# Kernel optimization log

Hardware: AMD Instinct MI355X
Metric: run time of the kernel (lower is better)

The kernel has to match this reference:

```python
import jax, jax.numpy as jnp
import numpy as np

DIM = 1024
HEAD_NUM = 8
D_HEAD = DIM // HEAD_NUM
B, S = 4, 2048


def setup_inputs() -> dict:
    key = jax.random.key(0)
    ks = jax.random.split(key, 7)
    scale = 0.02
    return {
        "Q": jax.random.normal(ks[0], (B, S, DIM), dtype=jnp.float32),
        "K": jax.random.normal(ks[1], (B, S, DIM), dtype=jnp.float32),
        "V": jax.random.normal(ks[2], (B, S, DIM), dtype=jnp.float32),
        "W_Q": jax.random.normal(ks[3], (DIM, DIM), dtype=jnp.float32) * scale,
        "W_K": jax.random.normal(ks[4], (DIM, DIM), dtype=jnp.float32) * scale,
        "W_V": jax.random.normal(ks[5], (DIM, DIM), dtype=jnp.float32) * scale,
        "W_O": jax.random.normal(ks[6], (DIM, DIM), dtype=jnp.float32) * scale,
    }


def reference(Q, K, V, W_Q, W_K, W_V, W_O):
    # torch nn.Linear(bias=False): y = x @ W.T
    b, s, d = Q.shape
    h, dh = HEAD_NUM, d // HEAD_NUM

    def proj_split(x, W):
        # split_head: tensor_split along feature dim into h contiguous chunks,
        # stack at dim 1 -> [b, h, s, dh]; equivalent to reshape+transpose.
        y = jnp.einsum('bsd,ed->bse', x, W)
        return y.reshape(b, s, h, dh).transpose(0, 2, 1, 3)

    q = proj_split(Q, W_Q)  # [b,h,s,dh]
    k = proj_split(K, W_K)
    v = proj_split(V, W_V)

    scores = jnp.einsum('bhqd,bhkd->bhqk', q, k) / jnp.sqrt(jnp.float32(dh))
    # FAITHFUL to original: nn.Softmax(dim=1) normalizes over the HEAD axis.
    attn = jax.nn.softmax(scores, axis=1)
    # dropout is identity in eval mode
    ctx = jnp.einsum('bhqk,bhkd->bhqd', attn, v)  # [b,h,s,dh]
    # concat_head: heads concatenated back along feature dim in order
    ctx = ctx.transpose(0, 2, 1, 3).reshape(b, s, d)
    return jnp.einsum('bsd,ed->bse', ctx, W_O)
```

## Files before the change

### kernel.cpp

```cpp
#include <hip/hip_runtime.h>
#include <math.h>
#include <stdint.h>


typedef __attribute__((ext_vector_type(8))) __bf16 bf16x8;
typedef __attribute__((ext_vector_type(4))) __bf16 bf16x4;
typedef __attribute__((ext_vector_type(4))) float  f32x4;

__device__ __forceinline__ f32x4 mfma16(bf16x8 a, bf16x8 b, f32x4 c) {
    return __builtin_amdgcn_mfma_f32_16x16x32_bf16(a, b, c, 0, 0, 0);
}

__device__ __forceinline__ void cp16(void* lds, const void* g) {
    __builtin_amdgcn_global_load_lds(
        (__attribute__((address_space(1))) void*)(void*)(const_cast<void*>(g)),
        (__attribute__((address_space(3))) void*)lds,
        16, 0, 0);
}

__global__ void cast_f32_to_bf16(const float* __restrict__ src,
                                 __bf16* __restrict__ dst, int n4) {
    int i = blockIdx.x * blockDim.x + threadIdx.x;
    const int stride = gridDim.x * blockDim.x;
    for (; i < n4; i += stride) {
        float4 f = ((const float4*)src)[i];
        bf16x4 o;
        o[0] = (__bf16)f.x; o[1] = (__bf16)f.y; o[2] = (__bf16)f.z; o[3] = (__bf16)f.w;
        ((bf16x4*)dst)[i] = o;
    }
}

__global__ void cast4_f32_to_bf16(const float* __restrict__ s0, __bf16* __restrict__ d0,
                                  const float* __restrict__ s1, __bf16* __restrict__ d1,
                                  const float* __restrict__ s2, __bf16* __restrict__ d2,
                                  const float* __restrict__ s3, __bf16* __restrict__ d3,
                                  int n4) {
    const float* s = (blockIdx.y == 0) ? s0 : (blockIdx.y == 1) ? s1
                    : (blockIdx.y == 2) ? s2 : s3;
    __bf16* d = (blockIdx.y == 0) ? d0 : (blockIdx.y == 1) ? d1
               : (blockIdx.y == 2) ? d2 : d3;
    int i = blockIdx.x * blockDim.x + threadIdx.x;
    const int stride = gridDim.x * blockDim.x;
    for (; i < n4; i += stride) {
        float4 f = ((const float4*)s)[i];
        bf16x4 o;
        o[0] = (__bf16)f.x; o[1] = (__bf16)f.y; o[2] = (__bf16)f.z; o[3] = (__bf16)f.w;
        ((bf16x4*)d)[i] = o;
    }
}

template<int MODE>
__global__ __launch_bounds__(256, 2) void gemm_bt(const __bf16* __restrict__ A,
                                                  const __bf16* __restrict__ Bt,
                                                  void* __restrict__ out,
                                                  float scale)
{
    __shared__ __bf16 As[128 * 32];
    __shared__ __bf16 Bs[128 * 32];
    const int tid  = threadIdx.x;
    const int lane = tid & 63;
    const int u = lane >> 4, v = lane & 15;
    const int w = tid >> 6;
    const int wm = (w >> 1) * 64, wn = (w & 1) * 64;
    const long tM = (long)blockIdx.y * 128;
    const int  tN = blockIdx.x * 128;

    f32x4 acc[4][4];
#pragma unroll
    for (int i = 0; i < 4; ++i)
#pragma unroll
        for (int j = 0; j < 4; ++j) acc[i][j] = (f32x4){0.f, 0.f, 0.f, 0.f};

    const int c0 = tid, c1 = tid + 256;
    const int ar0 = c0 >> 2, ak0 = (c0 & 3) * 8;
    const int ar1 = c1 >> 2, ak1 = (c1 & 3) * 8;

    const __bf16* Ab = A  + tM * 1024;
    const __bf16* Bb = Bt + (long)tN * 1024;

    for (int k0 = 0; k0 < 1024; k0 += 32) {
        __syncthreads();
        cp16(&As[ar0 * 32 + ak0], Ab + (long)ar0 * 1024 + k0 + ak0);
        cp16(&As[ar1 * 32 + ak1], Ab + (long)ar1 * 1024 + k0 + ak1);
        cp16(&Bs[ar0 * 32 + ak0], Bb + (long)ar0 * 1024 + k0 + ak0);
        cp16(&Bs[ar1 * 32 + ak1], Bb + (long)ar1 * 1024 + k0 + ak1);
        __syncthreads();

        bf16x8 af[4], bfr[4];
#pragma unroll
        for (int i = 0; i < 4; ++i)
            af[i] = *(const bf16x8*)&As[(wm + i * 16 + v) * 32 + u * 8];
#pragma unroll
        for (int j = 0; j < 4; ++j)
            bfr[j] = *(const bf16x8*)&Bs[(wn + j * 16 + v) * 32 + u * 8];
#pragma unroll
        for (int i = 0; i < 4; ++i)
#pragma unroll
            for (int j = 0; j < 4; ++j)
                acc[i][j] = mfma16(af[i], bfr[j], acc[i][j]);
    }

#pragma unroll
    for (int i = 0; i < 4; ++i) {
#pragma unroll
        for (int j = 0; j < 4; ++j) {
            const long row0 = tM + wm + i * 16 + u * 4;
            const int  col  = tN + wn + j * 16 + v;
            if (MODE == 0) {
                __bf16* o = (__bf16*)out;
#pragma unroll
                for (int r = 0; r < 4; ++r)
                    o[(row0 + r) * 1024 + col] = (__bf16)(acc[i][j][r] * scale);
            } else if (MODE == 1) {
                float* o = (float*)out;
#pragma unroll
                for (int r = 0; r < 4; ++r)
                    o[(row0 + r) * 1024 + col] = acc[i][j][r];
            } else {
                __bf16* o = (__bf16*)out;
                const int bidx = (int)(row0 >> 11);
                const int s    = (int)(row0 & 2047);
                const int h = col >> 7, dh = col & 127;
                bf16x4 pk;
#pragma unroll
                for (int r = 0; r < 4; ++r) pk[r] = (__bf16)acc[i][j][r];
                *(bf16x4*)&o[((long)(bidx * 8 + h) * 128 + dh) * 2048 + s] = pk;
            }
        }
    }
}

struct QkSm {
    union {
        struct { __bf16 As[64 * 32]; __bf16 Bs[128 * 32]; } s;
        __bf16 tb[128 * 68];
    };
};
__global__ __launch_bounds__(256, 2) void qk_head_softmax(
    const __bf16* __restrict__ kp, const __bf16* __restrict__ qp,
    __bf16* __restrict__ P, int b_base, int q_base)
{
    __shared__ QkSm sm;
    const int tid  = threadIdx.x;
    const int lane = tid & 63;
    const int u = lane >> 4, v = lane & 15;
    const int w = tid >> 6;
    const int wm = (w >> 1) * 32, wn = (w & 1) * 64;
    const int bloc = blockIdx.z;
    const int b    = b_base + bloc;
    const int k0   = blockIdx.x * 64;
    const int q0l  = blockIdx.y * 128;
    const int q0g  = q_base + q0l;
    const long Cq  = (long)gridDim.y * 128;

    const int ar0 = tid >> 2, ak0 = (tid & 3) * 8;
    const int ar1 = ar0 + 64, ak1 = ak0;

    const __bf16* Ka = kp + ((long)b * 2048 + k0) * 1024;
    const __bf16* Qa = qp + ((long)b * 2048 + q0g) * 1024;

    f32x4 den[2][4];
#pragma unroll
    for (int i = 0; i < 2; ++i)
#pragma unroll
        for (int j = 0; j < 4; ++j) den[i][j] = (f32x4){0.f, 0.f, 0.f, 0.f};

    bf16x4 e8[8][2][4];

#pragma unroll
    for (int h = 0; h < 8; ++h) {
        f32x4 acc[2][4];
#pragma unroll
        for (int i = 0; i < 2; ++i)
#pragma unroll
            for (int j = 0; j < 4; ++j) acc[i][j] = (f32x4){0.f, 0.f, 0.f, 0.f};

#pragma unroll
        for (int kb = 0; kb < 4; ++kb) {
            const int co = h * 128 + kb * 32;
            __syncthreads();
            cp16(&sm.s.As[ar0 * 32 + ak0], Ka + (long)ar0 * 1024 + co + ak0);
            cp16(&sm.s.Bs[ar0 * 32 + ak0], Qa + (long)ar0 * 1024 + co + ak0);
            cp16(&sm.s.Bs[ar1 * 32 + ak1], Qa + (long)ar1 * 1024 + co + ak1);
            __syncthreads();

            bf16x8 af[2], bfr[4];
#pragma unroll
            for (int i = 0; i < 2; ++i)
                af[i] = *(const bf16x8*)&sm.s.As[(wm + i * 16 + v) * 32 + u * 8];
#pragma unroll
            for (int j = 0; j < 4; ++j)
                bfr[j] = *(const bf16x8*)&sm.s.Bs[(wn + j * 16 + v) * 32 + u * 8];
#pragma unroll
            for (int i = 0; i < 2; ++i)
#pragma unroll
                for (int j = 0; j < 4; ++j)
                    acc[i][j] = mfma16(af[i], bfr[j], acc[i][j]);
        }
#pragma unroll
        for (int i = 0; i < 2; ++i)
#pragma unroll
            for (int j = 0; j < 4; ++j) {
                bf16x4 pk;
#pragma unroll
                for (int r = 0; r < 4; ++r) {
                    float e = __expf(acc[i][j][r]);
                    den[i][j][r] += e;
                    pk[r] = (__bf16)e;
                }
                e8[h][i][j] = pk;
            }
    }

    f32x4 rinv[2][4];
#pragma unroll
    for (int i = 0; i < 2; ++i)
#pragma unroll
        for (int j = 0; j < 4; ++j)
#pragma unroll
            for (int r = 0; r < 4; ++r) rinv[i][j][r] = 1.0f / den[i][j][r];

#pragma unroll
    for (int h = 0; h < 8; ++h) {
        __syncthreads();
#pragma unroll
        for (int i = 0; i < 2; ++i)
#pragma unroll
            for (int j = 0; j < 4; ++j) {
                const int kc = wm + i * 16 + u * 4;
                const int qr = wn + j * 16 + v;
                bf16x4 t = e8[h][i][j];
                bf16x4 o;
#pragma unroll
                for (int r = 0; r < 4; ++r)
                    o[r] = (__bf16)((float)t[r] * rinv[i][j][r]);
                *(bf16x4*)&sm.tb[qr * 68 + kc] = o;
            }
        __syncthreads();
        __bf16* Ph = P + ((long)(bloc * 8 + h) * Cq + q0l) * 2048 + k0;
#pragma unroll
        for (int p = 0; p < 4; ++p) {
            const int qq = p * 32 + (tid >> 3);
            const int kk = (tid & 7) * 8;
            *(bf16x8*)&Ph[(long)qq * 2048 + kk] = *(const bf16x8*)&sm.tb[qq * 68 + kk];
        }
    }
}

__global__ __launch_bounds__(256, 2) void pv_gemm(
    const __bf16* __restrict__ vt, const __bf16* __restrict__ P,
    __bf16* __restrict__ ctx, int b_base, int q_base)
{
    __shared__ __bf16 As[128 * 32];
    __shared__ __bf16 Bs[128 * 32];
    const int tid  = threadIdx.x;
    const int lane = tid & 63;
    const int u = lane >> 4, v = lane & 15;
    const int w = tid >> 6;
    const int wm = (w >> 1) * 64, wn = (w & 1) * 64;
    const int bhl  = blockIdx.y;
    const int bloc = bhl >> 3, h = bhl & 7;
    const int b    = b_base + bloc;
    const int q0l  = blockIdx.x * 128;
    const int q0g  = q_base + q0l;
    const long Cq  = (long)gridDim.x * 128;

    const int c0 = tid, c1 = tid + 256;
    const int ar0 = c0 >> 2, ak0 = (c0 & 3) * 8;
    const int ar1 = c1 >> 2, ak1 = (c1 & 3) * 8;

    const __bf16* Ab = vt + (long)(b * 8 + h) * 128 * 2048;
    const __bf16* Bb = P  + ((long)(bloc * 8 + h) * Cq + q0l) * 2048;

    f32x4 acc[4][4];
#pragma unroll
    for (int i = 0; i < 4; ++i)
#pragma unroll
        for (int j = 0; j < 4; ++j) acc[i][j] = (f32x4){0.f, 0.f, 0.f, 0.f};

    for (int k0 = 0; k0 < 2048; k0 += 32) {
        __syncthreads();
        cp16(&As[ar0 * 32 + ak0], Ab + (long)ar0 * 2048 + k0 + ak0);
        cp16(&As[ar1 * 32 + ak1], Ab + (long)ar1 * 2048 + k0 + ak1);
        cp16(&Bs[ar0 * 32 + ak0], Bb + (long)ar0 * 2048 + k0 + ak0);
        cp16(&Bs[ar1 * 32 + ak1], Bb + (long)ar1 * 2048 + k0 + ak1);
        __syncthreads();

        bf16x8 af[4], bfr[4];
#pragma unroll
        for (int i = 0; i < 4; ++i)
            af[i] = *(const bf16x8*)&As[(wm + i * 16 + v) * 32 + u * 8];
#pragma unroll
        for (int j = 0; j < 4; ++j)
            bfr[j] = *(const bf16x8*)&Bs[(wn + j * 16 + v) * 32 + u * 8];
#pragma unroll
        for (int i = 0; i < 4; ++i)
#pragma unroll
            for (int j = 0; j < 4; ++j)
                acc[i][j] = mfma16(af[i], bfr[j], acc[i][j]);
    }

#pragma unroll
    for (int i = 0; i < 4; ++i) {
#pragma unroll
        for (int j = 0; j < 4; ++j) {
            const int dh0 = wm + i * 16 + u * 4;
            const int q   = q0g + wn + j * 16 + v;
            bf16x4 pk;
#pragma unroll
            for (int r = 0; r < 4; ++r) pk[r] = (__bf16)acc[i][j][r];
            *(bf16x4*)&ctx[((long)b * 2048 + q) * 1024 + h * 128 + dh0] = pk;
        }
    }
}

__global__ __launch_bounds__(256, 2) void attn_softmax_head(
    const __bf16* __restrict__ qp, const __bf16* __restrict__ kp,
    const __bf16* __restrict__ vt, __bf16* __restrict__ ctx)
{
    __shared__ float part[8 * 256];
    __shared__ float pb[4][2][16 * 33];

    const int tid  = threadIdx.x;
    const int lane = tid & 63;
    const int w = tid >> 6;
    const int u = lane >> 4, v = lane & 15;
    const int b  = blockIdx.y;
    const int q0 = blockIdx.x * 16;

    const long qoff = ((long)b * 2048 + q0 + v) * 1024;
    bf16x8 qf[2][4];
#pragma unroll
    for (int hh = 0; hh < 2; ++hh) {
        const int h = 2 * w + hh;
#pragma unroll
        for (int kk = 0; kk < 4; ++kk)
            qf[hh][kk] = *(const bf16x8*)(qp + qoff + h * 128 + kk * 32 + u * 8);
    }

    f32x4 acc[2][8];
#pragma unroll
    for (int hh = 0; hh < 2; ++hh)
#pragma unroll
        for (int dt = 0; dt < 8; ++dt) acc[hh][dt] = (f32x4){0.f, 0.f, 0.f, 0.f};

    for (int kt = 0; kt < 2048; kt += 32) {
        float e[2][2][4];
#pragma unroll
        for (int hh = 0; hh < 2; ++hh) {
            const int h = 2 * w + hh;
#pragma unroll
            for (int t = 0; t < 2; ++t) {
                f32x4 s = (f32x4){0.f, 0.f, 0.f, 0.f};
                const __bf16* kb = kp + ((long)b * 2048 + kt + t * 16 + v) * 1024
                                      + h * 128 + u * 8;
#pragma unroll
                for (int kk = 0; kk < 4; ++kk)
                    s = mfma16(*(const bf16x8*)(kb + kk * 32), qf[hh][kk], s);
#pragma unroll
                for (int r = 0; r < 4; ++r) e[hh][t][r] = __expf(s[r]);
            }
        }
#pragma unroll
        for (int t = 0; t < 2; ++t)
#pragma unroll
            for (int r = 0; r < 4; ++r)
                part[(t * 4 + r) * 256 + w * 64 + lane] = e[0][t][r] + e[1][t][r];
        __syncthreads();
#pragma unroll
        for (int t = 0; t < 2; ++t)
#pragma unroll
            for (int r = 0; r < 4; ++r) {
                const int j = (t * 4 + r) * 256 + lane;
                const float den = part[j] + part[j + 64] + part[j + 128] + part[j + 192];
                const float rinv = 1.0f / den;
                const int kl = t * 16 + u * 4 + r;
                pb[w][0][v * 33 + kl] = e[0][t][r] * rinv;
                pb[w][1][v * 33 + kl] = e[1][t][r] * rinv;
            }
        bf16x8 pf[2];
#pragma unroll
        for (int hh = 0; hh < 2; ++hh)
#pragma unroll
            for (int jj = 0; jj < 8; ++jj)
                pf[hh][jj] = (__bf16)pb[w][hh][v * 33 + u * 8 + jj];
#pragma unroll
        for (int hh = 0; hh < 2; ++hh) {
            const int h = 2 * w + hh;
            const __bf16* vb = vt + ((long)(b * 8 + h) * 128 + v) * 2048 + kt + u * 8;
#pragma unroll
            for (int dt = 0; dt < 8; ++dt)
                acc[hh][dt] = mfma16(*(const bf16x8*)(vb + (long)dt * 16 * 2048),
                                     pf[hh], acc[hh][dt]);
        }
        __syncthreads();
    }

#pragma unroll
    for (int hh = 0; hh < 2; ++hh) {
        const int h = 2 * w + hh;
#pragma unroll
        for (int dt = 0; dt < 8; ++dt) {
            bf16x4 o;
#pragma unroll
            for (int r = 0; r < 4; ++r) o[r] = (__bf16)acc[hh][dt][r];
            *(bf16x4*)(ctx + ((long)b * 2048 + q0 + v) * 1024
                           + h * 128 + dt * 16 + u * 4) = o;
        }
    }
}

extern "C" void kernel_launch(void* const* d_in, const int* in_sizes, int n_in,
                              void* d_out, int out_size, void* d_ws, size_t ws_size,
                              hipStream_t stream)
{
    const float* Q  = (const float*)d_in[0];
    const float* K  = (const float*)d_in[1];
    const float* V  = (const float*)d_in[2];
    const float* WQ = (const float*)d_in[3];
    const float* WK = (const float*)d_in[4];
    const float* WV = (const float*)d_in[5];
    const float* WO = (const float*)d_in[6];

    __bf16* ws = (__bf16*)d_ws;
    __bf16* wq = ws;
    __bf16* wk = wq + 1048576;
    __bf16* wv = wk + 1048576;
    __bf16* wo = wv + 1048576;
    __bf16* xb = wo + 1048576;
    __bf16* qp = xb + 8388608;
    __bf16* kp = qp + 8388608;
    __bf16* vt = kp + 8388608;
    __bf16* pbuf = vt + 8388608;

    const float qscale = 0.08838834764831845f;

    cast4_f32_to_bf16<<<dim3(256, 4), 256, 0, stream>>>(
        WQ, wq, WK, wk, WV, wv, WO, wo, 262144);

    dim3 gg(8, 64), gb(256);
    cast_f32_to_bf16<<<4096, 256, 0, stream>>>(Q, xb, 2097152);
    gemm_bt<0><<<gg, gb, 0, stream>>>(xb, wq, qp, qscale);
    cast_f32_to_bf16<<<4096, 256, 0, stream>>>(K, xb, 2097152);
    gemm_bt<0><<<gg, gb, 0, stream>>>(xb, wk, kp, 1.0f);
    cast_f32_to_bf16<<<4096, 256, 0, stream>>>(V, xb, 2097152);
    gemm_bt<2><<<gg, gb, 0, stream>>>(xb, wv, vt, 1.0f);

    const size_t baseBytes = 37748736ULL * 2ULL;
    const size_t avail = (ws_size > baseBytes) ? ws_size - baseBytes : 0;
    const int cfgs[6][2] = {{4,2048},{2,2048},{1,2048},{1,1024},{1,512},{1,256}};
    int nb = 0, C = 0;
    for (int c = 0; c < 6; ++c) {
        const size_t need = (size_t)cfgs[c][0] * 8 * cfgs[c][1] * 2048 * 2;
        if (need <= avail) { nb = cfgs[c][0]; C = cfgs[c][1]; break; }
    }

    if (nb) {
        for (int bb = 0; bb < 4; bb += nb)
            for (int qq = 0; qq < 2048; qq += C) {
                qk_head_softmax<<<dim3(32, C / 128, nb), gb, 0, stream>>>(
                    kp, qp, pbuf, bb, qq);
                pv_gemm<<<dim3(C / 128, nb * 8), gb, 0, stream>>>(
                    vt, pbuf, xb, bb, qq);
            }
    } else {
        attn_softmax_head<<<dim3(128, 4), gb, 0, stream>>>(qp, kp, vt, xb);
    }

    gemm_bt<1><<<gg, gb, 0, stream>>>(xb, wo, (float*)d_out, 1.0f);
}
```

Before: 578.6 us.

## Recompute QK scores in second pass instead of holding exponentials in registers

The head-softmax kernel now runs the QK GEMM twice per head. The first pass only accumulates the softmax denominator, and the second pass recomputes the scores, exponentiates, normalizes and writes P. This drops the large per-thread e8 register array and raises the launch-bounds occupancy target from 2 to 4 blocks per CU. The shared-memory union is split into separate arrays and the head loops are no longer unrolled. The cost is double the QK MFMA work and double the global/LDS loads of Q and K tiles.

```diff
diff --git a/kernel.cpp b/kernel.cpp
--- a/kernel.cpp
+++ b/kernel.cpp
@@ -130,17 +130,13 @@
     }
 }
 
-struct QkSm {
-    union {
-        struct { __bf16 As[64 * 32]; __bf16 Bs[128 * 32]; } s;
-        __bf16 tb[128 * 68];
-    };
-};
-__global__ __launch_bounds__(256, 2) void qk_head_softmax(
+__global__ __launch_bounds__(256, 4) void qk_head_softmax(
     const __bf16* __restrict__ kp, const __bf16* __restrict__ qp,
     __bf16* __restrict__ P, int b_base, int q_base)
 {
-    __shared__ QkSm sm;
+    __shared__ __bf16 As[64 * 32];
+    __shared__ __bf16 Bs[128 * 32];
+    __shared__ __bf16 tb[128 * 68];
     const int tid  = threadIdx.x;
     const int lane = tid & 63;
     const int u = lane >> 4, v = lane & 15;
@@ -165,9 +161,7 @@
 #pragma unroll
         for (int j = 0; j < 4; ++j) den[i][j] = (f32x4){0.f, 0.f, 0.f, 0.f};
 
-    bf16x4 e8[8][2][4];
-
-#pragma unroll
+#pragma unroll 1
     for (int h = 0; h < 8; ++h) {
         f32x4 acc[2][4];
 #pragma unroll
@@ -179,18 +173,18 @@
         for (int kb = 0; kb < 4; ++kb) {
             const int co = h * 128 + kb * 32;
             __syncthreads();
-            cp16(&sm.s.As[ar0 * 32 + ak0], Ka + (long)ar0 * 1024 + co + ak0);
-            cp16(&sm.s.Bs[ar0 * 32 + ak0], Qa + (long)ar0 * 1024 + co + ak0);
-            cp16(&sm.s.Bs[ar1 * 32 + ak1], Qa + (long)ar1 * 1024 + co + ak1);
+            cp16(&As[ar0 * 32 + ak0], Ka + (long)ar0 * 1024 + co + ak0);
+            cp16(&Bs[ar0 * 32 + ak0], Qa + (long)ar0 * 1024 + co + ak0);
+            cp16(&Bs[ar1 * 32 + ak1], Qa + (long)ar1 * 1024 + co + ak1);
             __syncthreads();
 
             bf16x8 af[2], bfr[4];
 #pragma unroll
             for (int i = 0; i < 2; ++i)
-                af[i] = *(const bf16x8*)&sm.s.As[(wm + i * 16 + v) * 32 + u * 8];
+                af[i] = *(const bf16x8*)&As[(wm + i * 16 + v) * 32 + u * 8];
 #pragma unroll
             for (int j = 0; j < 4; ++j)
-                bfr[j] = *(const bf16x8*)&sm.s.Bs[(wn + j * 16 + v) * 32 + u * 8];
+                bfr[j] = *(const bf16x8*)&Bs[(wn + j * 16 + v) * 32 + u * 8];
 #pragma unroll
             for (int i = 0; i < 2; ++i)
 #pragma unroll
@@ -200,28 +194,49 @@
 #pragma unroll
         for (int i = 0; i < 2; ++i)
 #pragma unroll
-            for (int j = 0; j < 4; ++j) {
-                bf16x4 pk;
-#pragma unroll
-                for (int r = 0; r < 4; ++r) {
-                    float e = __expf(acc[i][j][r]);
-                    den[i][j][r] += e;
-                    pk[r] = (__bf16)e;
-                }
-                e8[h][i][j] = pk;
-            }
-    }
-
-    f32x4 rinv[2][4];
+            for (int j = 0; j < 4; ++j)
+#pragma unroll
+                for (int r = 0; r < 4; ++r)
+                    den[i][j][r] += __expf(acc[i][j][r]);
+    }
+
 #pragma unroll
     for (int i = 0; i < 2; ++i)
 #pragma unroll
         for (int j = 0; j < 4; ++j)
 #pragma unroll
-            for (int r = 0; r < 4; ++r) rinv[i][j][r] = 1.0f / den[i][j][r];
-
-#pragma unroll
+            for (int r = 0; r < 4; ++r) den[i][j][r] = 1.0f / den[i][j][r];
+
+#pragma unroll 1
     for (int h = 0; h < 8; ++h) {
+        f32x4 acc[2][4];
+#pragma unroll
+        for (int i = 0; i < 2; ++i)
+#pragma unroll
+            for (int j = 0; j < 4; ++j) acc[i][j] = (f32x4){0.f, 0.f, 0.f, 0.f};
+
+#pragma unroll
+        for (int kb = 0; kb < 4; ++kb) {
+            const int co = h * 128 + kb * 32;
+            __syncthreads();
+            cp16(&As[ar0 * 32 + ak0], Ka + (long)ar0 * 1024 + co + ak0);
+            cp16(&Bs[ar0 * 32 + ak0], Qa + (long)ar0 * 1024 + co + ak0);
+            cp16(&Bs[ar1 * 32 + ak1], Qa + (long)ar1 * 1024 + co + ak1);
+            __syncthreads();
+
+            bf16x8 af[2], bfr[4];
+#pragma unroll
+            for (int i = 0; i < 2; ++i)
+                af[i] = *(const bf16x8*)&As[(wm + i * 16 + v) * 32 + u * 8];
+#pragma unroll
+            for (int j = 0; j < 4; ++j)
+                bfr[j] = *(const bf16x8*)&Bs[(wn + j * 16 + v) * 32 + u * 8];
+#pragma unroll
+            for (int i = 0; i < 2; ++i)
+#pragma unroll
+                for (int j = 0; j < 4; ++j)
+                    acc[i][j] = mfma16(af[i], bfr[j], acc[i][j]);
+        }
         __syncthreads();
 #pragma unroll
         for (int i = 0; i < 2; ++i)
@@ -229,12 +244,13 @@
             for (int j = 0; j < 4; ++j) {
                 const int kc = wm + i * 16 + u * 4;
                 const int qr = wn + j * 16 + v;
-                bf16x4 t = e8[h][i][j];
                 bf16x4 o;
 #pragma unroll
-                for (int r = 0; r < 4; ++r)
-                    o[r] = (__bf16)((float)t[r] * rinv[i][j][r]);
-                *(bf16x4*)&sm.tb[qr * 68 + kc] = o;
+                for (int r = 0; r < 4; ++r) {
+                    float e = (float)(__bf16)__expf(acc[i][j][r]);
+                    o[r] = (__bf16)(e * den[i][j][r]);
+                }
+                *(bf16x4*)&tb[qr * 68 + kc] = o;
             }
         __syncthreads();
         __bf16* Ph = P + ((long)(bloc * 8 + h) * Cq + q0l) * 2048 + k0;
@@ -242,7 +258,7 @@
         for (int p = 0; p < 4; ++p) {
             const int qq = p * 32 + (tid >> 3);
             const int kk = (tid & 7) * 8;
-            *(bf16x8*)&Ph[(long)qq * 2048 + kk] = *(const bf16x8*)&sm.tb[qq * 68 + kk];
+            *(bf16x8*)&Ph[(long)qq * 2048 + kk] = *(const bf16x8*)&tb[qq * 68 + kk];
         }
     }
 }
```

New measurement: 505.6 us. 12.6% less time.
